# Optimization experiments

Hardware: AMD Instinct MI355X
Metric: run time of the kernel (lower is better)

Reference implementation:

```python
import jax, jax.numpy as jnp
import numpy as np

# dims: M scalars (0e), K vectors (1e) in input; T = tp_features; N = batch of atoms
M, K, T, N = 128, 64, 64, 131072
D_IN = M + 3 * K  # 320, e3nn layout: [128x0e | 64x1e flattened as (mul, 3)]


def _act_norm(f):
    # e3nn Activation normalizes act so E_{z~N(0,1)}[act(z)^2] = 1
    z = np.linspace(-8.0, 8.0, 20001)
    pdf = np.exp(-0.5 * z * z) / np.sqrt(2.0 * np.pi)
    return float(np.sqrt(np.trapz(f(z) ** 2 * pdf, z)))

C_SILU = _act_norm(lambda z: z / (1.0 + np.exp(-z)))
C_RELU = _act_norm(lambda z: np.maximum(z, 0.0))
INV_SQRT_M = float(1.0 / np.sqrt(M))
INV_SQRT_K = float(1.0 / np.sqrt(K))
INV_SQRT_3 = float(1.0 / np.sqrt(3.0))  # wigner_3j(1,1,0) = delta_ij/sqrt(3)
TP_NORM = float(1.0 / np.sqrt(2.0 * T * T))  # fan-in over the 2 paths into 0e


def setup_inputs() -> dict:
    key = jax.random.key(0)
    ks = jax.random.split(key, 11)
    f32 = jnp.float32
    return {
        "x": jax.random.normal(ks[0], (N, D_IN), f32),
        "input_shift": jnp.zeros((D_IN,), f32),
        "output_scale": jnp.ones((), f32),
        # PerceptronLayer 1: Linear (Mx0e+Kx1e) -> ((M+K)x0e + Kx1e)
        "w0_1": jax.random.normal(ks[1], (M, M + K), f32),
        "b0_1": jnp.zeros((M + K,), f32),
        "w1_1": jax.random.normal(ks[2], (K, K), f32),
        # PerceptronLayer 2 (same irreps, resnet applies)
        "w0_2": jax.random.normal(ks[3], (M, M + K), f32),
        "b0_2": jnp.zeros((M + K,), f32),
        "w1_2": jax.random.normal(ks[4], (K, K), f32),
        # linear_out: (Mx0e+Kx1e) -> (Tx0e+Tx1e)
        "w0_o": jax.random.normal(ks[5], (M, T), f32),
        "b0_o": jnp.zeros((T,), f32),
        "w1_o": jax.random.normal(ks[6], (K, T), f32),
        # FullyConnectedTensorProduct (tp, tp) -> 1x0e: paths 0e*0e->0e, 1e*1e->0e
        "w_tp0": jax.random.normal(ks[7], (T, T), f32),
        "w_tp1": jax.random.normal(ks[8], (T, T), f32),
    }


def _linear(xs, xv, w0, b0, w1):
    # e3nn o3.Linear: per-irrep dense mixing with 1/sqrt(fan_in), bias on 0e only
    ys = xs @ w0 * INV_SQRT_M + b0          # [N, M+K] scalars + gates
    yv = jnp.einsum('nki,kj->nji', xv, w1) * INV_SQRT_K  # [N, K, 3]
    return ys, yv


def _gate(ys, yv):
    # e3nn Gate: silu on 0e scalars, relu on 0e gates, gate the 1e vectors
    s = jax.nn.silu(ys[:, :M]) / C_SILU     # [N, M]
    g = jax.nn.relu(ys[:, M:]) / C_RELU     # [N, K]
    return s, yv * g[:, :, None]


def reference(x, input_shift, output_scale,
              w0_1, b0_1, w1_1, w0_2, b0_2, w1_2,
              w0_o, b0_o, w1_o, w_tp0, w_tp1):
    x = x - input_shift
    xs = x[:, :M]                           # [N, M] 0e block
    xv = x[:, M:].reshape(-1, K, 3)         # [N, K, 3] 1e block
    for (w0, b0, w1) in ((w0_1, b0_1, w1_1), (w0_2, b0_2, w1_2)):
        ys, yv = _linear(xs, xv, w0, b0, w1)
        s, v = _gate(ys, yv)
        xs = xs + s                         # resnet: irreps_in == irreps_out
        xv = xv + v
    # linear_out -> irreps_tp = Tx0e + Tx1e
    zs = xs @ w0_o * INV_SQRT_M + b0_o                    # [N, T]
    zv = jnp.einsum('nki,kj->nji', xv, w1_o) * INV_SQRT_K # [N, T, 3]
    # FullyConnectedTensorProduct(z, z) -> 0e (avoid [N,T,T] blowup)
    y0 = jnp.sum((zs @ w_tp0) * zs, axis=-1)                                    # [N]
    y1 = jnp.sum(jnp.einsum('nui,uv->nvi', zv, w_tp1) * zv, axis=(1, 2)) * INV_SQRT_3
    y = (y0 + y1) * TP_NORM / output_scale
    return y[:, None]
```

## Files before the change

kernel.cpp:

```cpp
#include <hip/hip_runtime.h>
#include <math.h>


typedef _Float16 f16;
typedef _Float16 f16x8 __attribute__((ext_vector_type(8)));
typedef __fp16   fp16x2 __attribute__((ext_vector_type(2)));
typedef float    f32x4 __attribute__((ext_vector_type(4)));
typedef int      i32x4 __attribute__((ext_vector_type(4)));

#define MFMA16(a, b, c) __builtin_amdgcn_mfma_f32_16x16x32_f16(a, b, c, 0, 0, 0)

constexpr float INV_SQRT_M = 0.08838834764831845f;
constexpr float INV_SQRT_K = 0.125f;
constexpr float INV_SQRT_3 = 0.57735026918962576f;
constexpr float TP_NORM    = 0.011048543456039806f;

#define OFF_W01 0
#define OFF_W11 24576
#define OFF_W02 28672
#define OFF_W12 53248
#define OFF_W0O 57344
#define OFF_W1O 65536
#define OFF_TP0 69632
#define OFF_TP1 73728
#define PACK_UNITS 9728
#define FB01 38912
#define FB02 39104
#define FB0O 39296
#define TOTAL_UNITS (PACK_UNITS + 448)

#define LDS_W1     24576
#define LDS_BIAS_F 14336
#define LDS_W0O    0
#define LDS_W1O    8192
#define LDS_TP0    12288
#define LDS_TP1    16384
#define LDS_B0O_F  10240

#define NTHR 512

__global__ void init_consts_kernel(float* __restrict__ ws) {
    __shared__ double red[1024];
    const int t = threadIdx.x;
    double acc_s = 0.0, acc_r = 0.0;
    for (int i = t; i <= 20000; i += 1024) {
        const double z = -8.0 + (16.0 * (double)i) / 20000.0;
        const double pdf = exp(-0.5 * z * z) / 2.5066282746310002;
        const double sil = z / (1.0 + exp(-z));
        const double wgt = (i == 0 || i == 20000) ? 0.5 : 1.0;
        acc_s += wgt * sil * sil * pdf;
        if (z > 0.0) acc_r += wgt * z * z * pdf;
    }
    red[t] = acc_s;
    __syncthreads();
    for (int o = 512; o > 0; o >>= 1) { if (t < o) red[t] += red[t + o]; __syncthreads(); }
    const double tot_s = red[0];
    __syncthreads();
    red[t] = acc_r;
    __syncthreads();
    for (int o = 512; o > 0; o >>= 1) { if (t < o) red[t] += red[t + o]; __syncthreads(); }
    if (t == 0) {
        const double dz = 16.0 / 20000.0;
        ws[0] = (float)(1.0 / sqrt(tot_s * dz));
        ws[1] = (float)(1.0 / sqrt(red[0] * dz));
    }
}

__global__ void pack_weights(const float* __restrict__ w01, const float* __restrict__ w11,
                             const float* __restrict__ w02, const float* __restrict__ w12,
                             const float* __restrict__ w0o, const float* __restrict__ w1o,
                             const float* __restrict__ tp0, const float* __restrict__ tp1,
                             const float* __restrict__ b01, const float* __restrict__ b02,
                             const float* __restrict__ b0o,
                             f16* __restrict__ dst) {
    int u = blockIdx.x * 256 + threadIdx.x;
    if (u >= TOTAL_UNITS) return;
    if (u >= PACK_UNITS) {
        const int idx = u - PACK_UNITS;
        float* dstF = (float*)dst;
        if (idx < 192)      dstF[FB01 + idx] = b01[idx];
        else if (idx < 384) dstF[FB02 + (idx - 192)] = b02[idx - 192];
        else                dstF[FB0O + (idx - 384)] = b0o[idx - 384];
        return;
    }
    const float* src; int NC, base, lu = u; float sc;
    if      (lu < 3072) {            src = w01; NC = 192; base = OFF_W01; sc = INV_SQRT_M; }
    else if (lu < 3584) { lu -= 3072; src = w11; NC = 64;  base = OFF_W11; sc = INV_SQRT_K; }
    else if (lu < 6656) { lu -= 3584; src = w02; NC = 192; base = OFF_W02; sc = INV_SQRT_M; }
    else if (lu < 7168) { lu -= 6656; src = w12; NC = 64;  base = OFF_W12; sc = INV_SQRT_K; }
    else if (lu < 8192) { lu -= 7168; src = w0o; NC = 64;  base = OFF_W0O; sc = INV_SQRT_M; }
    else if (lu < 8704) { lu -= 8192; src = w1o; NC = 64;  base = OFF_W1O; sc = INV_SQRT_K; }
    else if (lu < 9216) { lu -= 8704; src = tp0; NC = 64;  base = OFF_TP0; sc = 1.0f; }
    else                { lu -= 9216; src = tp1; NC = 64;  base = OFF_TP1; sc = INV_SQRT_3; }
    const int lane = lu & 63;
    const int frag = lu >> 6;
    const int NT = NC >> 4;
    const int kstep = frag / NT, nj = frag - kstep * NT;
    const int gl  = lane >> 4;
    const int col = nj * 16 + (lane & 15);
    f16 tmp[8];
    #pragma unroll
    for (int e = 0; e < 8; ++e) {
        const int row = kstep * 32 + ((e >> 2) << 4) + (gl << 2) + (e & 3);
        tmp[e] = (f16)(src[(size_t)row * NC + col] * sc);
    }
    *(f16x8*)&dst[(size_t)(base) + (size_t)lu * 8] = *(f16x8*)tmp;
}

__device__ __forceinline__ int pk2i(float a, float b) {
    union { fp16x2 h; int i; } u;
    u.h = __builtin_amdgcn_cvt_pkrtz(a, b);
    return u.i;
}

__device__ __forceinline__ f16x8 packB(f32x4 t0, f32x4 t1) {
    union { i32x4 i; f16x8 v; } u;
    u.i[0] = pk2i(t0[0], t0[1]);
    u.i[1] = pk2i(t0[2], t0[3]);
    u.i[2] = pk2i(t1[0], t1[1]);
    u.i[3] = pk2i(t1[2], t1[3]);
    return u.v;
}

union Frag { f16x8 v; fp16x2 h2[4]; };

__device__ __forceinline__ void resblock32(
    Frag (&xsS)[2][4], Frag (&xvS)[2][3][2],
    const f16* lds, float invCS, float invCR, int l, int g)
{
    const float* biasF = (const float*)lds + LDS_BIAS_F;

    f16x8 xsB[2][4];
    #pragma unroll
    for (int h = 0; h < 2; ++h)
        #pragma unroll
        for (int ks = 0; ks < 4; ++ks)
            xsB[h][ks] = xsS[h][ks].v;

    float gate[2][4][4];
    #pragma unroll
    for (int nj = 0; nj < 12; ++nj) {
        f32x4 acc0 = {0.f, 0.f, 0.f, 0.f}, acc1 = {0.f, 0.f, 0.f, 0.f};
        #pragma unroll
        for (int ks = 0; ks < 4; ++ks) {
            const f16x8 a = *(const f16x8*)&lds[(size_t)((ks * 12 + nj) * 64 + l) * 8];
            acc0 = MFMA16(a, xsB[0][ks], acc0);
            acc1 = MFMA16(a, xsB[1][ks], acc1);
        }
        const f32x4 bias = *(const f32x4*)&biasF[nj * 16 + g * 4];
        #pragma unroll
        for (int h = 0; h < 2; ++h) {
            const f32x4 acc = h ? acc1 : acc0;
            if (nj < 8) {
                float s[4];
                #pragma unroll
                for (int r = 0; r < 4; ++r) {
                    const float ys = acc[r] + bias[r];
                    s[r] = ys * __builtin_amdgcn_rcpf(1.0f + __expf(-ys)) * invCS;
                }
                xsS[h][nj >> 1].h2[2 * (nj & 1)]     += __builtin_amdgcn_cvt_pkrtz(s[0], s[1]);
                xsS[h][nj >> 1].h2[2 * (nj & 1) + 1] += __builtin_amdgcn_cvt_pkrtz(s[2], s[3]);
            } else {
                #pragma unroll
                for (int r = 0; r < 4; ++r) {
                    const float ys = acc[r] + bias[r];
                    gate[h][nj - 8][r] = fmaxf(ys, 0.f) * invCR;
                }
            }
        }
    }

    f16x8 xvB[2][3][2];
    #pragma unroll
    for (int h = 0; h < 2; ++h)
        #pragma unroll
        for (int i = 0; i < 3; ++i)
            #pragma unroll
            for (int ks = 0; ks < 2; ++ks)
                xvB[h][i][ks] = xvS[h][i][ks].v;

    #pragma unroll
    for (int i = 0; i < 3; ++i)
        #pragma unroll
        for (int nj = 0; nj < 4; ++nj) {
            f32x4 acc0 = {0.f, 0.f, 0.f, 0.f}, acc1 = {0.f, 0.f, 0.f, 0.f};
            #pragma unroll
            for (int ks = 0; ks < 2; ++ks) {
                const f16x8 a = *(const f16x8*)&lds[LDS_W1 + (size_t)((ks * 4 + nj) * 64 + l) * 8];
                acc0 = MFMA16(a, xvB[0][i][ks], acc0);
                acc1 = MFMA16(a, xvB[1][i][ks], acc1);
            }
            #pragma unroll
            for (int h = 0; h < 2; ++h) {
                const f32x4 acc = h ? acc1 : acc0;
                float u[4];
                #pragma unroll
                for (int r = 0; r < 4; ++r)
                    u[r] = acc[r] * gate[h][nj][r];
                xvS[h][i][nj >> 1].h2[2 * (nj & 1)]     += __builtin_amdgcn_cvt_pkrtz(u[0], u[1]);
                xvS[h][i][nj >> 1].h2[2 * (nj & 1) + 1] += __builtin_amdgcn_cvt_pkrtz(u[2], u[3]);
            }
        }
}

__global__ __launch_bounds__(NTHR, 2)
void corrnet_lds(const float* __restrict__ x, const float* __restrict__ shift,
                 const float* __restrict__ oscale,
                 const f16* __restrict__ wp, const float* __restrict__ consts,
                 float* __restrict__ out)
{
    __shared__ __align__(16) f16 smem[29056];
    float* smemF = (float*)smem;
    const float* wpF = (const float*)wp;

    const int t = threadIdx.x;
    const int l = t & 63;
    const int w = __builtin_amdgcn_readfirstlane(t >> 6);
    const int g = l >> 4;
    const int c = l & 15;
    const size_t n0 = (size_t)blockIdx.x * 256 + (size_t)w * 32;

    const float invCS = consts[0], invCR = consts[1];
    const float inv_os = 1.0f / oscale[0];

    #pragma unroll
    for (int it = 0; it < 7; ++it) {
        const int u = it * NTHR + t;
        *(f16x8*)&smem[(size_t)u * 8] = *(const f16x8*)&wp[(size_t)u * 8];
    }
    if (t < 48)
        ((f32x4*)&smemF[LDS_BIAS_F])[t] = ((const f32x4*)&wpF[FB01])[t];

    Frag xsS[2][4];
    Frag xvS[2][3][2];
    #pragma unroll
    for (int h = 0; h < 2; ++h) {
        const float* xrow = x + (n0 + h * 16 + c) * 320;
        #pragma unroll
        for (int ks = 0; ks < 4; ++ks) {
            const int col = ks * 32 + g * 4;
            const f32x4 t0 = *(const f32x4*)(xrow + col)      - *(const f32x4*)(shift + col);
            const f32x4 t1 = *(const f32x4*)(xrow + col + 16) - *(const f32x4*)(shift + col + 16);
            xsS[h][ks].v = packB(t0, t1);
        }
        f32x4 tmp[3][4];
        #pragma unroll
        for (int tau = 0; tau < 4; ++tau) {
            const int col = 128 + 3 * (tau * 16 + g * 4);
            const f32x4 a0 = *(const f32x4*)(xrow + col)     - *(const f32x4*)(shift + col);
            const f32x4 a1 = *(const f32x4*)(xrow + col + 4) - *(const f32x4*)(shift + col + 4);
            const f32x4 a2 = *(const f32x4*)(xrow + col + 8) - *(const f32x4*)(shift + col + 8);
            float arr[12];
            #pragma unroll
            for (int e = 0; e < 4; ++e) {
                arr[e] = a0[e]; arr[4 + e] = a1[e]; arr[8 + e] = a2[e];
            }
            #pragma unroll
            for (int r = 0; r < 4; ++r)
                #pragma unroll
                for (int i = 0; i < 3; ++i)
                    tmp[i][tau][r] = arr[3 * r + i];
        }
        #pragma unroll
        for (int i = 0; i < 3; ++i)
            #pragma unroll
            for (int ks = 0; ks < 2; ++ks)
                xvS[h][i][ks].v = packB(tmp[i][2 * ks], tmp[i][2 * ks + 1]);
    }

    __syncthreads();
    resblock32(xsS, xvS, smem, invCS, invCR, l, g);
    __syncthreads();

    #pragma unroll
    for (int it = 0; it < 7; ++it) {
        const int u = it * NTHR + t;
        *(f16x8*)&smem[(size_t)u * 8] = *(const f16x8*)&wp[(size_t)(OFF_W02) + (size_t)u * 8];
    }
    if (t < 48)
        ((f32x4*)&smemF[LDS_BIAS_F])[t] = ((const f32x4*)&wpF[FB02])[t];
    __syncthreads();
    resblock32(xsS, xvS, smem, invCS, invCR, l, g);
    __syncthreads();

    #pragma unroll
    for (int it = 0; it < 5; ++it) {
        const int u = it * NTHR + t;
        *(f16x8*)&smem[(size_t)u * 8] = *(const f16x8*)&wp[(size_t)(OFF_W0O) + (size_t)u * 8];
    }
    if (t < 16)
        ((f32x4*)&smemF[LDS_B0O_F])[t] = ((const f32x4*)&wpF[FB0O])[t];
    __syncthreads();

    f32x4 zs[2][4];
    #pragma unroll
    for (int nj = 0; nj < 4; ++nj) {
        f32x4 acc0 = {0.f, 0.f, 0.f, 0.f}, acc1 = {0.f, 0.f, 0.f, 0.f};
        #pragma unroll
        for (int ks = 0; ks < 4; ++ks) {
            const f16x8 a = *(const f16x8*)&smem[LDS_W0O + (size_t)((ks * 4 + nj) * 64 + l) * 8];
            acc0 = MFMA16(a, xsS[0][ks].v, acc0);
            acc1 = MFMA16(a, xsS[1][ks].v, acc1);
        }
        const f32x4 bias = *(const f32x4*)&smemF[LDS_B0O_F + nj * 16 + g * 4];
        #pragma unroll
        for (int r = 0; r < 4; ++r) {
            zs[0][nj][r] = acc0[r] + bias[r];
            zs[1][nj][r] = acc1[r] + bias[r];
        }
    }

    float part[2]  = {0.f, 0.f};
    float part1[2] = {0.f, 0.f};

    {
        f16x8 zsB[2][2];
        #pragma unroll
        for (int h = 0; h < 2; ++h)
            #pragma unroll
            for (int ks = 0; ks < 2; ++ks)
                zsB[h][ks] = packB(zs[h][2 * ks], zs[h][2 * ks + 1]);
        #pragma unroll
        for (int nj = 0; nj < 4; ++nj) {
            f32x4 acc0 = {0.f, 0.f, 0.f, 0.f}, acc1 = {0.f, 0.f, 0.f, 0.f};
            #pragma unroll
            for (int ks = 0; ks < 2; ++ks) {
                const f16x8 a = *(const f16x8*)&smem[LDS_TP0 + (size_t)((ks * 4 + nj) * 64 + l) * 8];
                acc0 = MFMA16(a, zsB[0][ks], acc0);
                acc1 = MFMA16(a, zsB[1][ks], acc1);
            }
            #pragma unroll
            for (int r = 0; r < 4; ++r) {
                part[0] += acc0[r] * zs[0][nj][r];
                part[1] += acc1[r] * zs[1][nj][r];
            }
        }
    }

    #pragma unroll
    for (int i = 0; i < 3; ++i) {
        f32x4 zv[2][4];
        #pragma unroll
        for (int nj = 0; nj < 4; ++nj) {
            f32x4 acc0 = {0.f, 0.f, 0.f, 0.f}, acc1 = {0.f, 0.f, 0.f, 0.f};
            #pragma unroll
            for (int ks = 0; ks < 2; ++ks) {
                const f16x8 a = *(const f16x8*)&smem[LDS_W1O + (size_t)((ks * 4 + nj) * 64 + l) * 8];
                acc0 = MFMA16(a, xvS[0][i][ks].v, acc0);
                acc1 = MFMA16(a, xvS[1][i][ks].v, acc1);
            }
            #pragma unroll
            for (int r = 0; r < 4; ++r) {
                zv[0][nj][r] = acc0[r];
                zv[1][nj][r] = acc1[r];
            }
        }
        f16x8 zvB[2][2];
        #pragma unroll
        for (int h = 0; h < 2; ++h)
            #pragma unroll
            for (int ks = 0; ks < 2; ++ks)
                zvB[h][ks] = packB(zv[h][2 * ks], zv[h][2 * ks + 1]);
        #pragma unroll
        for (int nj = 0; nj < 4; ++nj) {
            f32x4 acc0 = {0.f, 0.f, 0.f, 0.f}, acc1 = {0.f, 0.f, 0.f, 0.f};
            #pragma unroll
            for (int ks = 0; ks < 2; ++ks) {
                const f16x8 a = *(const f16x8*)&smem[LDS_TP1 + (size_t)((ks * 4 + nj) * 64 + l) * 8];
                acc0 = MFMA16(a, zvB[0][ks], acc0);
                acc1 = MFMA16(a, zvB[1][ks], acc1);
            }
            #pragma unroll
            for (int r = 0; r < 4; ++r) {
                part1[0] += acc0[r] * zv[0][nj][r];
                part1[1] += acc1[r] * zv[1][nj][r];
            }
        }
    }
    #pragma unroll
    for (int h = 0; h < 2; ++h)
        part[h] += part1[h];

    #pragma unroll
    for (int h = 0; h < 2; ++h) {
        part[h] += __shfl_xor(part[h], 16, 64);
        part[h] += __shfl_xor(part[h], 32, 64);
    }

    if (l < 16)
        out[n0 + l] = part[0] * TP_NORM * inv_os;
    else if (l < 32)
        out[n0 + 16 + (l - 16)] = part[1] * TP_NORM * inv_os;
}

extern "C" void kernel_launch(void* const* d_in, const int* in_sizes, int n_in,
                              void* d_out, int out_size, void* d_ws, size_t ws_size,
                              hipStream_t stream) {
    const float* x      = (const float*)d_in[0];
    const float* shift  = (const float*)d_in[1];
    const float* oscale = (const float*)d_in[2];
    const float* w01    = (const float*)d_in[3];
    const float* b01    = (const float*)d_in[4];
    const float* w11    = (const float*)d_in[5];
    const float* w02    = (const float*)d_in[6];
    const float* b02    = (const float*)d_in[7];
    const float* w12    = (const float*)d_in[8];
    const float* w0o    = (const float*)d_in[9];
    const float* b0o    = (const float*)d_in[10];
    const float* w1o    = (const float*)d_in[11];
    const float* wtp0   = (const float*)d_in[12];
    const float* wtp1   = (const float*)d_in[13];
    float* out    = (float*)d_out;
    float* consts = (float*)d_ws;
    f16*   wp     = (f16*)((char*)d_ws + 16);

    init_consts_kernel<<<1, 1024, 0, stream>>>(consts);
    pack_weights<<<(TOTAL_UNITS + 255) / 256, 256, 0, stream>>>(
        w01, w11, w02, w12, w0o, w1o, wtp0, wtp1, b01, b02, b0o, wp);

    const int nblocks = 131072 / 256;
    corrnet_lds<<<nblocks, NTHR, 0, stream>>>(
        x, shift, oscale, wp, consts, out);
}
```

Measured before the change: 75.65 us.

## Prefetch next-stage weights into registers during compute and raise MFMA wave priority

Weights for the second residual block and the output linear are now loaded from global memory into registers before the preceding resblock runs. They are written to LDS only after the following barrier, so their global-load latency overlaps with MFMA work instead of stalling between stages. MFMA loops are wrapped in s_setprio raises to favour matrix-issuing waves. The launch bound is relaxed from 2 to 1 waves-per-EU hint, allowing more registers for the prefetch buffers at the risk of lower occupancy.

```diff
diff --git a/kernel.cpp b/kernel.cpp
--- a/kernel.cpp
+++ b/kernel.cpp
@@ -141,12 +141,14 @@
     #pragma unroll
     for (int nj = 0; nj < 12; ++nj) {
         f32x4 acc0 = {0.f, 0.f, 0.f, 0.f}, acc1 = {0.f, 0.f, 0.f, 0.f};
+        __builtin_amdgcn_s_setprio(1);
         #pragma unroll
         for (int ks = 0; ks < 4; ++ks) {
             const f16x8 a = *(const f16x8*)&lds[(size_t)((ks * 12 + nj) * 64 + l) * 8];
             acc0 = MFMA16(a, xsB[0][ks], acc0);
             acc1 = MFMA16(a, xsB[1][ks], acc1);
         }
+        __builtin_amdgcn_s_setprio(0);
         const f32x4 bias = *(const f32x4*)&biasF[nj * 16 + g * 4];
         #pragma unroll
         for (int h = 0; h < 2; ++h) {
@@ -184,12 +186,14 @@
         #pragma unroll
         for (int nj = 0; nj < 4; ++nj) {
             f32x4 acc0 = {0.f, 0.f, 0.f, 0.f}, acc1 = {0.f, 0.f, 0.f, 0.f};
+            __builtin_amdgcn_s_setprio(1);
             #pragma unroll
             for (int ks = 0; ks < 2; ++ks) {
                 const f16x8 a = *(const f16x8*)&lds[LDS_W1 + (size_t)((ks * 4 + nj) * 64 + l) * 8];
                 acc0 = MFMA16(a, xvB[0][i][ks], acc0);
                 acc1 = MFMA16(a, xvB[1][i][ks], acc1);
             }
+            __builtin_amdgcn_s_setprio(0);
             #pragma unroll
             for (int h = 0; h < 2; ++h) {
                 const f32x4 acc = h ? acc1 : acc0;
@@ -203,7 +207,7 @@
         }
 }
 
-__global__ __launch_bounds__(NTHR, 2)
+__global__ __launch_bounds__(NTHR, 1)
 void corrnet_lds(const float* __restrict__ x, const float* __restrict__ shift,
                  const float* __restrict__ oscale,
                  const f16* __restrict__ wp, const float* __restrict__ consts,
@@ -269,39 +273,55 @@
     }
 
     __syncthreads();
+
+    f16x8 pf1[7];
+    f32x4 pfb1;
+    #pragma unroll
+    for (int it = 0; it < 7; ++it)
+        pf1[it] = *(const f16x8*)&wp[(size_t)(OFF_W02) + (size_t)(it * NTHR + t) * 8];
+    if (t < 48)
+        pfb1 = ((const f32x4*)&wpF[FB02])[t];
+
     resblock32(xsS, xvS, smem, invCS, invCR, l, g);
     __syncthreads();
 
     #pragma unroll
-    for (int it = 0; it < 7; ++it) {
-        const int u = it * NTHR + t;
-        *(f16x8*)&smem[(size_t)u * 8] = *(const f16x8*)&wp[(size_t)(OFF_W02) + (size_t)u * 8];
-    }
+    for (int it = 0; it < 7; ++it)
+        *(f16x8*)&smem[(size_t)(it * NTHR + t) * 8] = pf1[it];
     if (t < 48)
-        ((f32x4*)&smemF[LDS_BIAS_F])[t] = ((const f32x4*)&wpF[FB02])[t];
+        ((f32x4*)&smemF[LDS_BIAS_F])[t] = pfb1;
+
+    f16x8 pf2[5];
+    f32x4 pfb2;
+    #pragma unroll
+    for (int it = 0; it < 5; ++it)
+        pf2[it] = *(const f16x8*)&wp[(size_t)(OFF_W0O) + (size_t)(it * NTHR + t) * 8];
+    if (t < 16)
+        pfb2 = ((const f32x4*)&wpF[FB0O])[t];
+
     __syncthreads();
     resblock32(xsS, xvS, smem, invCS, invCR, l, g);
     __syncthreads();
 
     #pragma unroll
-    for (int it = 0; it < 5; ++it) {
-        const int u = it * NTHR + t;
-        *(f16x8*)&smem[(size_t)u * 8] = *(const f16x8*)&wp[(size_t)(OFF_W0O) + (size_t)u * 8];
-    }
+    for (int it = 0; it < 5; ++it)
+        *(f16x8*)&smem[(size_t)(it * NTHR + t) * 8] = pf2[it];
     if (t < 16)
-        ((f32x4*)&smemF[LDS_B0O_F])[t] = ((const f32x4*)&wpF[FB0O])[t];
+        ((f32x4*)&smemF[LDS_B0O_F])[t] = pfb2;
     __syncthreads();
 
     f32x4 zs[2][4];
     #pragma unroll
     for (int nj = 0; nj < 4; ++nj) {
         f32x4 acc0 = {0.f, 0.f, 0.f, 0.f}, acc1 = {0.f, 0.f, 0.f, 0.f};
+        __builtin_amdgcn_s_setprio(1);
         #pragma unroll
         for (int ks = 0; ks < 4; ++ks) {
             const f16x8 a = *(const f16x8*)&smem[LDS_W0O + (size_t)((ks * 4 + nj) * 64 + l) * 8];
             acc0 = MFMA16(a, xsS[0][ks].v, acc0);
             acc1 = MFMA16(a, xsS[1][ks].v, acc1);
         }
+        __builtin_amdgcn_s_setprio(0);
         const f32x4 bias = *(const f32x4*)&smemF[LDS_B0O_F + nj * 16 + g * 4];
         #pragma unroll
         for (int r = 0; r < 4; ++r) {
@@ -323,12 +343,14 @@
         #pragma unroll
         for (int nj = 0; nj < 4; ++nj) {
             f32x4 acc0 = {0.f, 0.f, 0.f, 0.f}, acc1 = {0.f, 0.f, 0.f, 0.f};
+            __builtin_amdgcn_s_setprio(1);
             #pragma unroll
             for (int ks = 0; ks < 2; ++ks) {
                 const f16x8 a = *(const f16x8*)&smem[LDS_TP0 + (size_t)((ks * 4 + nj) * 64 + l) * 8];
                 acc0 = MFMA16(a, zsB[0][ks], acc0);
                 acc1 = MFMA16(a, zsB[1][ks], acc1);
             }
+            __builtin_amdgcn_s_setprio(0);
             #pragma unroll
             for (int r = 0; r < 4; ++r) {
                 part[0] += acc0[r] * zs[0][nj][r];
@@ -343,12 +365,14 @@
         #pragma unroll
         for (int nj = 0; nj < 4; ++nj) {
             f32x4 acc0 = {0.f, 0.f, 0.f, 0.f}, acc1 = {0.f, 0.f, 0.f, 0.f};
+            __builtin_amdgcn_s_setprio(1);
             #pragma unroll
             for (int ks = 0; ks < 2; ++ks) {
                 const f16x8 a = *(const f16x8*)&smem[LDS_W1O + (size_t)((ks * 4 + nj) * 64 + l) * 8];
                 acc0 = MFMA16(a, xvS[0][i][ks].v, acc0);
                 acc1 = MFMA16(a, xvS[1][i][ks].v, acc1);
             }
+            __builtin_amdgcn_s_setprio(0);
             #pragma unroll
             for (int r = 0; r < 4; ++r) {
                 zv[0][nj][r] = acc0[r];
@@ -364,12 +388,14 @@
         #pragma unroll
         for (int nj = 0; nj < 4; ++nj) {
             f32x4 acc0 = {0.f, 0.f, 0.f, 0.f}, acc1 = {0.f, 0.f, 0.f, 0.f};
+            __builtin_amdgcn_s_setprio(1);
             #pragma unroll
             for (int ks = 0; ks < 2; ++ks) {
                 const f16x8 a = *(const f16x8*)&smem[LDS_TP1 + (size_t)((ks * 4 + nj) * 64 + l) * 8];
                 acc0 = MFMA16(a, zvB[0][ks], acc0);
                 acc1 = MFMA16(a, zvB[1][ks], acc1);
             }
+            __builtin_amdgcn_s_setprio(0);
             #pragma unroll
             for (int r = 0; r < 4; ++r) {
                 part1[0] += acc0[r] * zv[0][nj][r];
```

Result: slower. 101.8 us (+34.5%).

## Preload all packed weights into LDS once and drop inter-stage reloads

Applied to the files above, without the earlier changes.

Loads every packed weight matrix and bias into one large shared-memory buffer at kernel start, removing the per-layer reload phases and their barriers. The LDS footprint grows to about 157 KB per block, so launch bounds drop to one block per CU. This trades fewer barriers and reloads for halved occupancy and more weight traffic per block.

```diff
diff --git a/kernel.cpp b/kernel.cpp
--- a/kernel.cpp
+++ b/kernel.cpp
@@ -27,15 +27,7 @@
 #define FB01 38912
 #define FB02 39104
 #define FB0O 39296
-#define TOTAL_UNITS (PACK_UNITS + 448)
-
-#define LDS_W1     24576
-#define LDS_BIAS_F 14336
-#define LDS_W0O    0
-#define LDS_W1O    8192
-#define LDS_TP0    12288
-#define LDS_TP1    16384
-#define LDS_B0O_F  10240
+#define TOTAL_UNITS 9840
 
 #define NTHR 512
 
@@ -74,7 +66,7 @@
                              const float* __restrict__ b0o,
                              f16* __restrict__ dst) {
     int u = blockIdx.x * 256 + threadIdx.x;
-    if (u >= TOTAL_UNITS) return;
+    if (u >= PACK_UNITS + 448) return;
     if (u >= PACK_UNITS) {
         const int idx = u - PACK_UNITS;
         float* dstF = (float*)dst;
@@ -126,10 +118,9 @@
 
 __device__ __forceinline__ void resblock32(
     Frag (&xsS)[2][4], Frag (&xvS)[2][3][2],
-    const f16* lds, float invCS, float invCR, int l, int g)
+    const f16* w0p, const float* biasF,
+    float invCS, float invCR, int l, int g)
 {
-    const float* biasF = (const float*)lds + LDS_BIAS_F;
-
     f16x8 xsB[2][4];
     #pragma unroll
     for (int h = 0; h < 2; ++h)
@@ -143,7 +134,7 @@
         f32x4 acc0 = {0.f, 0.f, 0.f, 0.f}, acc1 = {0.f, 0.f, 0.f, 0.f};
         #pragma unroll
         for (int ks = 0; ks < 4; ++ks) {
-            const f16x8 a = *(const f16x8*)&lds[(size_t)((ks * 12 + nj) * 64 + l) * 8];
+            const f16x8 a = *(const f16x8*)&w0p[(size_t)((ks * 12 + nj) * 64 + l) * 8];
             acc0 = MFMA16(a, xsB[0][ks], acc0);
             acc1 = MFMA16(a, xsB[1][ks], acc1);
         }
@@ -186,7 +177,7 @@
             f32x4 acc0 = {0.f, 0.f, 0.f, 0.f}, acc1 = {0.f, 0.f, 0.f, 0.f};
             #pragma unroll
             for (int ks = 0; ks < 2; ++ks) {
-                const f16x8 a = *(const f16x8*)&lds[LDS_W1 + (size_t)((ks * 4 + nj) * 64 + l) * 8];
+                const f16x8 a = *(const f16x8*)&w0p[24576 + (size_t)((ks * 4 + nj) * 64 + l) * 8];
                 acc0 = MFMA16(a, xvB[0][i][ks], acc0);
                 acc1 = MFMA16(a, xvB[1][i][ks], acc1);
             }
@@ -203,33 +194,33 @@
         }
 }
 
-__global__ __launch_bounds__(NTHR, 2)
+__global__ __launch_bounds__(NTHR, 1)
 void corrnet_lds(const float* __restrict__ x, const float* __restrict__ shift,
                  const float* __restrict__ oscale,
                  const f16* __restrict__ wp, const float* __restrict__ consts,
                  float* __restrict__ out)
 {
-    __shared__ __align__(16) f16 smem[29056];
+    __shared__ __align__(16) f16 smem[TOTAL_UNITS * 8];
     float* smemF = (float*)smem;
-    const float* wpF = (const float*)wp;
 
     const int t = threadIdx.x;
     const int l = t & 63;
-    const int w = __builtin_amdgcn_readfirstlane(t >> 6);
     const int g = l >> 4;
     const int c = l & 15;
-    const size_t n0 = (size_t)blockIdx.x * 256 + (size_t)w * 32;
+    const size_t n0 = (size_t)blockIdx.x * 256 + (size_t)(t >> 6) * 32;
 
     const float invCS = consts[0], invCR = consts[1];
     const float inv_os = 1.0f / oscale[0];
 
     #pragma unroll
-    for (int it = 0; it < 7; ++it) {
+    for (int it = 0; it < 19; ++it) {
         const int u = it * NTHR + t;
         *(f16x8*)&smem[(size_t)u * 8] = *(const f16x8*)&wp[(size_t)u * 8];
     }
-    if (t < 48)
-        ((f32x4*)&smemF[LDS_BIAS_F])[t] = ((const f32x4*)&wpF[FB01])[t];
+    if (t < 112) {
+        const int u = 19 * NTHR + t;
+        *(f16x8*)&smem[(size_t)u * 8] = *(const f16x8*)&wp[(size_t)u * 8];
+    }
 
     Frag xsS[2][4];
     Frag xvS[2][3][2];
@@ -269,28 +260,9 @@
     }
 
     __syncthreads();
-    resblock32(xsS, xvS, smem, invCS, invCR, l, g);
-    __syncthreads();
-
-    #pragma unroll
-    for (int it = 0; it < 7; ++it) {
-        const int u = it * NTHR + t;
-        *(f16x8*)&smem[(size_t)u * 8] = *(const f16x8*)&wp[(size_t)(OFF_W02) + (size_t)u * 8];
-    }
-    if (t < 48)
-        ((f32x4*)&smemF[LDS_BIAS_F])[t] = ((const f32x4*)&wpF[FB02])[t];
-    __syncthreads();
-    resblock32(xsS, xvS, smem, invCS, invCR, l, g);
-    __syncthreads();
-
-    #pragma unroll
-    for (int it = 0; it < 5; ++it) {
-        const int u = it * NTHR + t;
-        *(f16x8*)&smem[(size_t)u * 8] = *(const f16x8*)&wp[(size_t)(OFF_W0O) + (size_t)u * 8];
-    }
-    if (t < 16)
-        ((f32x4*)&smemF[LDS_B0O_F])[t] = ((const f32x4*)&wpF[FB0O])[t];
-    __syncthreads();
+
+    resblock32(xsS, xvS, smem + OFF_W01, smemF + FB01, invCS, invCR, l, g);
+    resblock32(xsS, xvS, smem + OFF_W02, smemF + FB02, invCS, invCR, l, g);
 
     f32x4 zs[2][4];
     #pragma unroll
@@ -298,11 +270,11 @@
         f32x4 acc0 = {0.f, 0.f, 0.f, 0.f}, acc1 = {0.f, 0.f, 0.f, 0.f};
         #pragma unroll
         for (int ks = 0; ks < 4; ++ks) {
-            const f16x8 a = *(const f16x8*)&smem[LDS_W0O + (size_t)((ks * 4 + nj) * 64 + l) * 8];
+            const f16x8 a = *(const f16x8*)&smem[OFF_W0O + (size_t)((ks * 4 + nj) * 64 + l) * 8];
             acc0 = MFMA16(a, xsS[0][ks].v, acc0);
             acc1 = MFMA16(a, xsS[1][ks].v, acc1);
         }
-        const f32x4 bias = *(const f32x4*)&smemF[LDS_B0O_F + nj * 16 + g * 4];
+        const f32x4 bias = *(const f32x4*)&smemF[FB0O + nj * 16 + g * 4];
         #pragma unroll
         for (int r = 0; r < 4; ++r) {
             zs[0][nj][r] = acc0[r] + bias[r];
@@ -325,7 +297,7 @@
             f32x4 acc0 = {0.f, 0.f, 0.f, 0.f}, acc1 = {0.f, 0.f, 0.f, 0.f};
             #pragma unroll
             for (int ks = 0; ks < 2; ++ks) {
-                const f16x8 a = *(const f16x8*)&smem[LDS_TP0 + (size_t)((ks * 4 + nj) * 64 + l) * 8];
+                const f16x8 a = *(const f16x8*)&smem[OFF_TP0 + (size_t)((ks * 4 + nj) * 64 + l) * 8];
                 acc0 = MFMA16(a, zsB[0][ks], acc0);
                 acc1 = MFMA16(a, zsB[1][ks], acc1);
             }
@@ -345,7 +317,7 @@
             f32x4 acc0 = {0.f, 0.f, 0.f, 0.f}, acc1 = {0.f, 0.f, 0.f, 0.f};
             #pragma unroll
             for (int ks = 0; ks < 2; ++ks) {
-                const f16x8 a = *(const f16x8*)&smem[LDS_W1O + (size_t)((ks * 4 + nj) * 64 + l) * 8];
+                const f16x8 a = *(const f16x8*)&smem[OFF_W1O + (size_t)((ks * 4 + nj) * 64 + l) * 8];
                 acc0 = MFMA16(a, xvS[0][i][ks].v, acc0);
                 acc1 = MFMA16(a, xvS[1][i][ks].v, acc1);
             }
@@ -366,7 +338,7 @@
             f32x4 acc0 = {0.f, 0.f, 0.f, 0.f}, acc1 = {0.f, 0.f, 0.f, 0.f};
             #pragma unroll
             for (int ks = 0; ks < 2; ++ks) {
-                const f16x8 a = *(const f16x8*)&smem[LDS_TP1 + (size_t)((ks * 4 + nj) * 64 + l) * 8];
+                const f16x8 a = *(const f16x8*)&smem[OFF_TP1 + (size_t)((ks * 4 + nj) * 64 + l) * 8];
                 acc0 = MFMA16(a, zvB[0][ks], acc0);
                 acc1 = MFMA16(a, zvB[1][ks], acc1);
             }
@@ -415,7 +387,7 @@
     f16*   wp     = (f16*)((char*)d_ws + 16);
 
     init_consts_kernel<<<1, 1024, 0, stream>>>(consts);
-    pack_weights<<<(TOTAL_UNITS + 255) / 256, 256, 0, stream>>>(
+    pack_weights<<<(PACK_UNITS + 448 + 255) / 256, 256, 0, stream>>>(
         w01, w11, w02, w12, w0o, w1o, wtp0, wtp1, b01, b02, b0o, wp);
 
     const int nblocks = 131072 / 256;
```

Result: slower. 81.61 us (+7.9%).
